# Kernel tuning notes

Measured on AMD Instinct MI355X. Metric: run time of the kernel, lower is better.

Reference implementation:

```python
import jax, jax.numpy as jnp
import numpy as np

SR = 16000
NUM_MEL = 80
FRAME_LEN = 400
FRAME_SHIFT = 160
PADDED_WIN = 512         # next pow2 of 400
NUM_FFT_BINS = PADDED_WIN // 2 + 1  # 257
PREEMPH = 0.97
EPS = 1e-6


def _mel_scale(f):
    return 1127.0 * np.log(1.0 + f / 700.0)


def _get_mel_banks(num_bins, window_padded, sample_freq, low_freq=20.0, high_freq=0.0):
    # Faithful port of torchaudio.compliance.kaldi.get_mel_banks (vtln_warp=1.0)
    num_fft_bins = window_padded // 2  # 256 (last bin padded with zero later)
    nyquist = 0.5 * sample_freq
    if high_freq <= 0.0:
        high_freq = nyquist + high_freq
    fft_bin_width = sample_freq / window_padded
    mel_low = _mel_scale(low_freq)
    mel_high = _mel_scale(high_freq)
    mel_delta = (mel_high - mel_low) / (num_bins + 1)
    left = mel_low + np.arange(num_bins, dtype=np.float64)[:, None] * mel_delta
    center = left + mel_delta
    right = center + mel_delta
    mel = _mel_scale(fft_bin_width * np.arange(num_fft_bins, dtype=np.float64))[None, :]
    up = (mel - left) / (center - left)
    down = (right - mel) / (right - center)
    bins = np.maximum(0.0, np.minimum(up, down))
    return bins.astype(np.float32)  # [num_bins, window_padded//2]


def _make_buffers():
    n = np.arange(FRAME_LEN, dtype=np.float32)
    window = (0.54 - 0.46 * np.cos(2 * np.pi * n / (FRAME_LEN - 1))).astype(np.float32)
    t = np.arange(PADDED_WIN, dtype=np.float32)
    f = np.arange(NUM_FFT_BINS, dtype=np.float32)[:, None]
    angles = 2.0 * np.pi * f * t / PADDED_WIN
    dft_real = np.cos(angles).astype(np.float32)        # [257, 512]
    dft_imag = (-np.sin(angles)).astype(np.float32)     # [257, 512]
    mel = _get_mel_banks(NUM_MEL, PADDED_WIN, float(SR))
    mel_weight = np.pad(mel, ((0, 0), (0, 1)))          # [80, 257]
    return window, dft_real, dft_imag, mel_weight


def setup_inputs() -> dict:
    key = jax.random.key(0)
    waveform = jax.random.normal(key, (32, 480000), dtype=jnp.float32)
    window, dft_real, dft_imag, mel_weight = _make_buffers()
    return {
        "waveform": waveform,
        "window": jnp.asarray(window),
        "dft_real": jnp.asarray(dft_real),
        "dft_imag": jnp.asarray(dft_imag),
        "mel_weight": jnp.asarray(mel_weight),
    }


def reference(waveform, window, dft_real, dft_imag, mel_weight):
    B, T = waveform.shape
    num_frames = (T - FRAME_LEN) // FRAME_SHIFT + 1
    # Framing (equivalent to conv1d with identity kernel, stride=FRAME_SHIFT)
    idx = jnp.arange(num_frames)[:, None] * FRAME_SHIFT + jnp.arange(FRAME_LEN)
    frames = waveform[:, idx].reshape(B * num_frames, FRAME_LEN)  # [BF, 400]
    # dither == 0 -> skipped
    # remove DC offset
    frames = frames - jnp.mean(frames, axis=1, keepdims=True)
    # raw energy (computed by the original module; unused since use_energy=False)
    _log_energy = jnp.log(jnp.maximum(jnp.sum(frames * frames, axis=1), EPS))
    # preemphasis with replicate left pad
    prev = jnp.concatenate([frames[:, :1], frames[:, :-1]], axis=1)
    frames = frames - PREEMPH * prev
    # Hamming window + zero pad to 512
    frames = frames * window[None, :]
    frames = jnp.pad(frames, ((0, 0), (0, PADDED_WIN - FRAME_LEN)))  # [BF, 512]
    # Brute-force DFT as matmuls
    real = frames @ dft_real.T  # [BF, 257]
    imag = frames @ dft_imag.T  # [BF, 257]
    power = real * real + imag * imag
    # Mel projection + log
    mel = power @ mel_weight.T + EPS  # [BF, 80]
    mel = jnp.log(jnp.maximum(mel, EPS))
    return mel.reshape(B, num_frames, NUM_MEL)
```

## Files before the change

### kernel.cpp

```cpp
#include <hip/hip_runtime.h>
#include <math.h>


#define BATCH 32
#define TLEN 480000
#define NFRAMES 2998
#define FL 400
#define FS 160
#define PW 512
#define NM 80
#define MT 32
#define NTILES 94
#define PRE 0.97f
#define EPSF 1e-6f

#define RE_KS 9
#define IM_KS 8
#define RE_U16 (16 * RE_KS * 64 * 8)
#define IM_U16 (16 * IM_KS * 64 * 8)
#define MEL_U16 (6 * 8 * 64 * 8)
#define OFF_REH 0
#define OFF_REL RE_U16
#define OFF_IMH (2 * RE_U16)
#define OFF_IML (2 * RE_U16 + IM_U16)
#define OFF_MEL (2 * RE_U16 + 2 * IM_U16)
#define WS_NEED ((size_t)(OFF_MEL + MEL_U16) * 2)

#define C0_SH 0
#define C0_SL 8704
#define C0_DH 17408
#define C0_DL 26112
#define C1_SH 0
#define C1_SL 10240
#define C1_DH 20480
#define C1_DL 29184

typedef short bf16x8 __attribute__((ext_vector_type(8)));
typedef float f32x4 __attribute__((ext_vector_type(4)));
typedef unsigned int u32;
typedef unsigned short u16;
typedef u32 u32x4 __attribute__((ext_vector_type(4)));

__device__ __forceinline__ u16 f2bf(float f) {
    u32 u = __builtin_bit_cast(u32, f);
    return (u16)((u + 0x7FFFu + ((u >> 16) & 1u)) >> 16);
}
__device__ __forceinline__ float bf2f(u16 h) {
    u32 u = ((u32)h) << 16;
    return __builtin_bit_cast(float, u);
}

__global__ void prep_kernel(const float* __restrict__ dftr, const float* __restrict__ dfti,
                            const float* __restrict__ melw, u16* __restrict__ wsb) {
    int idx = blockIdx.x * 256 + threadIdx.x;
    if (idx < 16 * RE_KS * 64) {
        int nf = idx / (RE_KS * 64);
        int rem = idx - nf * (RE_KS * 64);
        int ks = rem >> 6, l = rem & 63;
        int f = nf * 16 + (l & 15);
        int k = ks * 32 + ((l >> 4) << 3);
        u16* dh = wsb + OFF_REH + (size_t)idx * 8;
        u16* dl = wsb + OFF_REL + (size_t)idx * 8;
        #pragma unroll
        for (int e = 0; e < 8; ++e) {
            int kk = k + e;
            float x = (kk <= 256) ? dftr[(size_t)f * PW + kk] : 0.f;
            u16 h = f2bf(x);
            dh[e] = h;
            dl[e] = f2bf(x - bf2f(h));
        }
    } else if (idx < 16 * RE_KS * 64 + 16 * IM_KS * 64) {
        int j = idx - 16 * RE_KS * 64;
        int nf = j / (IM_KS * 64);
        int rem = j - nf * (IM_KS * 64);
        int ks = rem >> 6, l = rem & 63;
        int f = nf * 16 + (l & 15);
        int k = ks * 32 + ((l >> 4) << 3);
        u16* dh = wsb + OFF_IMH + (size_t)j * 8;
        u16* dl = wsb + OFF_IML + (size_t)j * 8;
        #pragma unroll
        for (int e = 0; e < 8; ++e) {
            float x = dfti[(size_t)f * PW + k + e];
            u16 h = f2bf(x);
            dh[e] = h;
            dl[e] = f2bf(x - bf2f(h));
        }
    } else {
        int m = idx - (16 * RE_KS * 64 + 16 * IM_KS * 64);
        if (m < 6 * 8 * 64) {
            int nf = m / (8 * 64);
            int ks = (m >> 6) & 7, l = m & 63;
            int n = nf * 16 + (l & 15);
            int k = ks * 32 + ((l >> 4) << 3);
            u16* dst = wsb + OFF_MEL + (size_t)m * 8;
            #pragma unroll
            for (int e = 0; e < 8; ++e)
                dst[e] = (n < NM) ? f2bf(melw[(size_t)n * 257 + k + e]) : (u16)0;
        }
    }
}

__device__ __forceinline__ u32 swz(int SWT, u32 r) {
    return (SWT == 0) ? ((r & 7u) << 4) : (SWT == 1) ? (((r >> 1) & 3u) << 4) : 0u;
}

#define MFMA6(D, J)                                                                        \
    _Pragma("unroll")                                                                      \
    for (int mf = 0; mf < 2; ++mf) {                                                       \
        acc[mf][J] = __builtin_amdgcn_mfma_f32_16x16x32_bf16(aH[mf], D[0], acc[mf][J], 0, 0, 0); \
        acc[mf][J] = __builtin_amdgcn_mfma_f32_16x16x32_bf16(aL[mf], D[0], acc[mf][J], 0, 0, 0); \
        acc[mf][J] = __builtin_amdgcn_mfma_f32_16x16x32_bf16(aH[mf], D[1], acc[mf][J], 0, 0, 0); \
    }

template<int RS, int SWT, int NKS, int BKS>
__device__ __forceinline__ void dft_pass(
    const char* tH, const char* tL,
    const u16* __restrict__ bH, const u16* __restrict__ bL,
    int ks0, int g, int lane, f32x4 (&acc)[2][4]) {

    bf16x8 aH[2], aL[2], Ba[2], Bb[2];

#define LDA_P(KS)                                                              \
    { _Pragma("unroll")                                                        \
      for (int mf = 0; mf < 2; ++mf) {                                         \
        u32 r = (u32)(mf * 16 + (lane & 15));                                  \
        u32 off = (u32)((KS) * 64 + ((lane >> 4) << 4));                       \
        u32 byte = r * RS + (off ^ swz(SWT, r));                               \
        aH[mf] = *(const bf16x8*)(tH + byte);                                  \
        aL[mf] = *(const bf16x8*)(tL + byte);                                  \
      } }
#define LDB_P(KSG, J, D)                                                       \
    {                                                                          \
        size_t o = ((size_t)((4 * g + (J)) * BKS + (KSG)) * 64 + lane) * 8;    \
        D[0] = *(const bf16x8*)(bH + o);                                       \
        D[1] = *(const bf16x8*)(bL + o);                                       \
    }

    LDB_P(ks0, 0, Ba);
    #pragma unroll
    for (int ks = 0; ks < NKS; ++ks) {
        LDA_P(ks);
        LDB_P(ks0 + ks, 1, Bb);
        MFMA6(Ba, 0);
        LDB_P(ks0 + ks, 2, Ba);
        MFMA6(Bb, 1);
        LDB_P(ks0 + ks, 3, Bb);
        MFMA6(Ba, 2);
        if (ks + 1 < NKS) LDB_P(ks0 + ks + 1, 0, Ba);
        MFMA6(Bb, 3);
    }
#undef LDA_P
#undef LDB_P
}

__device__ __forceinline__ void pack_write(const float* ys, char* baseH, char* baseL, u32 byte) {
    u32x4 hv, lv;
    #pragma unroll
    for (int e = 0; e < 4; ++e) {
        u16 h0 = f2bf(ys[2 * e]), h1 = f2bf(ys[2 * e + 1]);
        hv[e] = (u32)h0 | ((u32)h1 << 16);
        u16 l0 = f2bf(ys[2 * e] - bf2f(h0)), l1 = f2bf(ys[2 * e + 1] - bf2f(h1));
        lv[e] = (u32)l0 | ((u32)l1 << 16);
    }
    *(u32x4*)(baseH + byte) = hv;
    *(u32x4*)(baseL + byte) = lv;
}

__global__ __launch_bounds__(256, 3) void fbank_mfma(
    const float* __restrict__ wave, const float* __restrict__ win,
    const u16* __restrict__ wsb, float* __restrict__ out) {
    __shared__ float smean[MT];
    __shared__ u16 stile[18944];
    char* T = (char*)stile;

    const int tid = threadIdx.x, w = tid >> 6, lane = tid & 63;
    const int q = lane >> 4;
    const int cg = lane & 15;
    const int b = blockIdx.y;
    const int f0 = blockIdx.x * MT;
    const float* wb = wave + (size_t)b * TLEN;
    const float4* win4 = (const float4*)win;

    float mean[2];
    #pragma unroll
    for (int i = 0; i < 2; ++i) {
        const int rr = w * 8 + i * 4 + q;
        const int fr = f0 + rr;
        float acc = 0.f;
        if (fr < NFRAMES) {
            const float4* x4 = (const float4*)(wb + (size_t)fr * FS);
            #pragma unroll
            for (int m = 0; m < 6; ++m) {
                float4 a = x4[cg + 16 * m];
                acc += a.x + a.y + a.z + a.w;
            }
            if (cg < 4) { float4 a = x4[96 + cg]; acc += a.x + a.y + a.z + a.w; }
        }
        #pragma unroll
        for (int o = 8; o; o >>= 1) acc += __shfl_xor(acc, o);
        mean[i] = acc * (1.0f / FL);
        if (cg == 0) smean[rr] = mean[i];
    }

    #pragma unroll
    for (int i = 0; i < 2; ++i) {
        const int rr = w * 8 + i * 4 + q;
        const int fr = f0 + rr;
        const bool valid = fr < NFRAMES;
        const float* x = wb + (size_t)fr * FS;
        const float4* x4 = (const float4*)x;
        const float mc = (1.0f - PRE) * mean[i];

        float4 v0 = {0,0,0,0}, v1 = {0,0,0,0};
        if (valid) { v0 = x4[2 * cg]; v1 = x4[2 * cg + 1]; }
        float4 w0 = win4[2 * cg], w1 = win4[2 * cg + 1];
        float xpn = __shfl(v1.w, lane - 1);
        float xprev = (cg == 0) ? v0.x : xpn;
        float y[8];
        y[0] = (v0.x - PRE * xprev - mc) * w0.x;
        y[1] = (v0.y - PRE * v0.x - mc) * w0.y;
        y[2] = (v0.z - PRE * v0.y - mc) * w0.z;
        y[3] = (v0.w - PRE * v0.z - mc) * w0.w;
        y[4] = (v1.x - PRE * v0.w - mc) * w1.x;
        y[5] = (v1.y - PRE * v1.x - mc) * w1.y;
        y[6] = (v1.z - PRE * v1.y - mc) * w1.z;
        y[7] = (v1.w - PRE * v1.z - mc) * w1.w;

        float yr[8];
        #pragma unroll
        for (int e = 0; e < 8; ++e) yr[e] = 0.f;
        if (cg >= 14) {
            const int u0 = 512 - 8 * cg;
            float4 xr0 = {0,0,0,0}, xr1 = {0,0,0,0};
            float xu0 = 0.f;
            if (valid) {
                xr0 = x4[u0 / 4 - 2]; xr1 = x4[u0 / 4 - 1];
                if (u0 <= 399) xu0 = x[u0];
            }
            float4 wr0 = win4[u0 / 4 - 2], wr1 = win4[u0 / 4 - 1];
            float wu0 = (u0 <= 399) ? win[u0] : 0.f;
            yr[0] = (xu0   - PRE * xr1.w - mc) * wu0;
            yr[1] = (xr1.w - PRE * xr1.z - mc) * wr1.w;
            yr[2] = (xr1.z - PRE * xr1.y - mc) * wr1.z;
            yr[3] = (xr1.y - PRE * xr1.x - mc) * wr1.y;
            yr[4] = (xr1.x - PRE * xr0.w - mc) * wr1.x;
            yr[5] = (xr0.w - PRE * xr0.z - mc) * wr0.w;
            yr[6] = (xr0.z - PRE * xr0.y - mc) * wr0.z;
            yr[7] = (xr0.y - PRE * xr0.x - mc) * wr0.y;
        }
        float s8[8], d8[8];
        #pragma unroll
        for (int e = 0; e < 8; ++e) { s8[e] = y[e] + yr[e]; d8[e] = y[e] - yr[e]; }
        u32 byte = (u32)rr * 272u + (u32)cg * 16u;
        pack_write(s8, T + C0_SH, T + C0_SL, byte);
        pack_write(d8, T + C0_DH, T + C0_DL, byte);
    }
    __syncthreads();

    const int g = w;
    f32x4 accR[2][4], accI[2][4];
    #pragma unroll
    for (int mf = 0; mf < 2; ++mf)
        #pragma unroll
        for (int j = 0; j < 4; ++j) { accR[mf][j] = (f32x4)0.f; accI[mf][j] = (f32x4)0.f; }

    dft_pass<272, 2, 4, RE_KS>(T + C0_SH, T + C0_SL, wsb + OFF_REH, wsb + OFF_REL, 0, g, lane, accR);
    dft_pass<272, 2, 4, IM_KS>(T + C0_DH, T + C0_DL, wsb + OFF_IMH, wsb + OFF_IML, 0, g, lane, accI);
    __syncthreads();

    #pragma unroll
    for (int i = 0; i < 2; ++i) {
        const int rr = w * 8 + i * 4 + q;
        const int fr = f0 + rr;
        const bool valid = fr < NFRAMES;
        const float* x = wb + (size_t)fr * FS;
        const float4* x4 = (const float4*)x;
        const float mc = (1.0f - PRE) * mean[i];

        float4 v0 = {0,0,0,0}, v1 = {0,0,0,0};
        if (valid) { v0 = x4[32 + 2 * cg]; v1 = x4[33 + 2 * cg]; }
        float4 w0 = win4[32 + 2 * cg], w1 = win4[33 + 2 * cg];
        float xpn = __shfl(v1.w, lane - 1);
        float xprev = (cg == 0) ? (valid ? x[127] : 0.f) : xpn;
        float y[8];
        y[0] = (v0.x - PRE * xprev - mc) * w0.x;
        y[1] = (v0.y - PRE * v0.x - mc) * w0.y;
        y[2] = (v0.z - PRE * v0.y - mc) * w0.z;
        y[3] = (v0.w - PRE * v0.z - mc) * w0.w;
        y[4] = (v1.x - PRE * v0.w - mc) * w1.x;
        y[5] = (v1.y - PRE * v1.x - mc) * w1.y;
        y[6] = (v1.z - PRE * v1.y - mc) * w1.z;
        y[7] = (v1.w - PRE * v1.z - mc) * w1.w;

        const int u0 = 384 - 8 * cg;
        float4 xr0 = {0,0,0,0}, xr1 = {0,0,0,0};
        float xu0 = 0.f;
        if (valid) { xr0 = x4[u0 / 4 - 2]; xr1 = x4[u0 / 4 - 1]; xu0 = x[u0]; }
        float4 wr0 = win4[u0 / 4 - 2], wr1 = win4[u0 / 4 - 1];
        float wu0 = win[u0];
        float yr[8];
        yr[0] = (xu0   - PRE * xr1.w - mc) * wu0;
        yr[1] = (xr1.w - PRE * xr1.z - mc) * wr1.w;
        yr[2] = (xr1.z - PRE * xr1.y - mc) * wr1.z;
        yr[3] = (xr1.y - PRE * xr1.x - mc) * wr1.y;
        yr[4] = (xr1.x - PRE * xr0.w - mc) * wr1.x;
        yr[5] = (xr0.w - PRE * xr0.z - mc) * wr0.w;
        yr[6] = (xr0.z - PRE * xr0.y - mc) * wr0.z;
        yr[7] = (xr0.y - PRE * xr0.x - mc) * wr0.y;

        float s8[8], d8[8];
        #pragma unroll
        for (int e = 0; e < 8; ++e) { s8[e] = y[e] + yr[e]; d8[e] = y[e] - yr[e]; }
        u32 byteS = (u32)rr * 320u + (((u32)cg * 16u) ^ ((((u32)rr >> 1) & 3u) << 4));
        u32 byteD = (u32)rr * 272u + (u32)cg * 16u;
        pack_write(s8, T + C1_SH, T + C1_SL, byteS);
        pack_write(d8, T + C1_DH, T + C1_DL, byteD);
    }
    {
        const int rr = tid & 31;
        const int grp = tid >> 5;
        if (grp < 4) {
            const int fr = f0 + rr;
            float y256 = 0.f;
            if (grp == 0 && fr < NFRAMES) {
                const float* x = wb + (size_t)fr * FS;
                y256 = (x[256] - PRE * x[255] - (1.0f - PRE) * smean[rr]) * win[256];
            }
            float s8[8] = {y256, 0.f, 0.f, 0.f, 0.f, 0.f, 0.f, 0.f};
            u32 byte = (u32)rr * 320u + ((((u32)(16 + grp)) * 16u) ^ ((((u32)rr >> 1) & 3u) << 4));
            pack_write(s8, T + C1_SH, T + C1_SL, byte);
        }
    }
    __syncthreads();

    dft_pass<320, 1, 5, RE_KS>(T + C1_SH, T + C1_SL, wsb + OFF_REH, wsb + OFF_REL, 4, g, lane, accR);
    dft_pass<272, 2, 4, IM_KS>(T + C1_DH, T + C1_DL, wsb + OFF_IMH, wsb + OFF_IML, 4, g, lane, accI);
    __syncthreads();

    #pragma unroll
    for (int mf = 0; mf < 2; ++mf)
        #pragma unroll
        for (int j = 0; j < 4; ++j)
            #pragma unroll
            for (int r = 0; r < 4; ++r) {
                float pR = accR[mf][j][r], pI = accI[mf][j][r];
                float pw = pR * pR + pI * pI;
                u32 row = (u32)(mf * 16 + (q << 2) + r);
                u32 bin = (u32)(64 * g + j * 16 + cg);
                u32 byte = (row * 512u + bin * 2u) ^ ((row & 7u) << 4);
                *(u16*)(T + byte) = f2bf(pw);
            }
    __syncthreads();

    const u16* melb = wsb + OFF_MEL;
    {
        const int mfm = w >> 1;
        const int nf0 = (w & 1) ? 3 : 0;
        f32x4 accM[3];
        #pragma unroll
        for (int j = 0; j < 3; ++j) accM[j] = (f32x4)0.f;
        for (int ks = 0; ks < 8; ++ks) {
            u32 row = (u32)(mfm * 16 + cg);
            u32 byte = (row * 512u + (u32)(ks * 32 + (q << 3)) * 2u) ^ ((row & 7u) << 4);
            bf16x8 aP = *(const bf16x8*)(T + byte);
            #pragma unroll
            for (int j = 0; j < 3; ++j) {
                bf16x8 bM = *(const bf16x8*)(melb + ((size_t)((nf0 + j) * 8 + ks) * 64 + lane) * 8);
                accM[j] = __builtin_amdgcn_mfma_f32_16x16x32_bf16(aP, bM, accM[j], 0, 0, 0);
            }
        }
        #pragma unroll
        for (int j = 0; j < 3; ++j) {
            const int m = (nf0 + j) * 16 + cg;
            #pragma unroll
            for (int r = 0; r < 4; ++r) {
                const int rowl = mfm * 16 + (q << 2) + r;
                const int fr = f0 + rowl;
                if (fr < NFRAMES && m < NM) {
                    float v = fmaxf(accM[j][r] + EPSF, EPSF);
                    out[((size_t)b * NFRAMES + fr) * NM + m] = logf(v);
                }
            }
        }
    }
}

#define TFB 16
#define NB 256
__global__ __launch_bounds__(256, 3) void fbank_fallback(
    const float* __restrict__ wave, const float* __restrict__ win,
    const float* __restrict__ dftr, const float* __restrict__ dfti,
    const float* __restrict__ melw, float* __restrict__ out) {
    __shared__ float s_fr[TFB][PW];
    __shared__ float s_pw[TFB][NB + 1];
    const int tid = threadIdx.x, wv = tid >> 6, lane = tid & 63;
    const int fbase = blockIdx.x * TFB;
    #pragma unroll
    for (int j = 0; j < TFB / 4; ++j) {
        const int lf = wv * (TFB / 4) + j;
        const int gid = fbase + lf;
        const int bb = gid / NFRAMES;
        const int fr = gid - bb * NFRAMES;
        const float* x = wave + (size_t)bb * TLEN + (size_t)fr * FS;
        float s = 0.f;
        for (int i = lane; i < FL; i += 64) s += x[i];
        #pragma unroll
        for (int off = 32; off >= 1; off >>= 1) s += __shfl_xor(s, off);
        const float mean = s * (1.0f / FL);
        for (int i = lane; i < FL; i += 64) {
            const float xi = x[i];
            const float xm = (i == 0) ? xi : x[i - 1];
            s_fr[lf][i] = (xi - PRE * xm - (1.0f - PRE) * mean) * win[i];
        }
        for (int i = FL + lane; i < PW; i += 64) s_fr[lf][i] = 0.f;
    }
    __syncthreads();
    {
        const int bin = tid;
        const float4* dr4 = (const float4*)(dftr + (size_t)bin * PW);
        const float4* di4 = (const float4*)(dfti + (size_t)bin * PW);
        float accr[TFB], acci[TFB];
        #pragma unroll
        for (int f = 0; f < TFB; ++f) { accr[f] = 0.f; acci[f] = 0.f; }
        for (int k4 = 0; k4 < PW / 4; ++k4) {
            const float4 r = dr4[k4], im = di4[k4];
            #pragma unroll
            for (int f = 0; f < TFB; ++f) {
                const float4 fr = *(const float4*)&s_fr[f][k4 * 4];
                accr[f] += fr.x * r.x + fr.y * r.y + fr.z * r.z + fr.w * r.w;
                acci[f] += fr.x * im.x + fr.y * im.y + fr.z * im.z + fr.w * im.w;
            }
        }
        #pragma unroll
        for (int f = 0; f < TFB; ++f) s_pw[f][bin] = accr[f] * accr[f] + acci[f] * acci[f];
    }
    __syncthreads();
    for (int o = tid; o < TFB * NM; o += 256) {
        const int f = o / NM, m = o - f * NM;
        const float* wm = melw + (size_t)m * 257;
        float acc = 0.f;
        for (int k = 0; k < NB; ++k) acc += s_pw[f][k] * wm[k];
        out[(size_t)(fbase + f) * NM + m] = logf(fmaxf(acc + EPSF, EPSF));
    }
}

extern "C" void kernel_launch(void* const* d_in, const int* in_sizes, int n_in,
                              void* d_out, int out_size, void* d_ws, size_t ws_size,
                              hipStream_t stream) {
    const float* wave = (const float*)d_in[0];
    const float* win  = (const float*)d_in[1];
    const float* dftr = (const float*)d_in[2];
    const float* dfti = (const float*)d_in[3];
    const float* melw = (const float*)d_in[4];
    float* out = (float*)d_out;

    if (ws_size >= WS_NEED) {
        u16* wsb = (u16*)d_ws;
        const int prep_threads = 16 * RE_KS * 64 + 16 * IM_KS * 64 + 6 * 8 * 64;
        prep_kernel<<<(prep_threads + 255) / 256, 256, 0, stream>>>(dftr, dfti, melw, wsb);
        dim3 grid(NTILES, BATCH);
        fbank_mfma<<<grid, 256, 0, stream>>>(wave, win, wsb, out);
    } else {
        const int nblocks = (BATCH * NFRAMES) / TFB;
        fbank_fallback<<<nblocks, 256, 0, stream>>>(wave, win, dftr, dfti, melw, out);
    }
}
```

Measured before the change: 126.3 us.

## Apply DC-offset removal in frequency domain via precomputed window-DFT correction

Instead of a separate pass over each frame to compute the mean before preemphasis, the frame sum is accumulated from the samples already loaded for the DFT staging. Mean subtraction is applied after the DFT by subtracting mean times a precomputed DFT of the window, computed in the prep kernel. This removes a second global read of each frame before the DFT. In exchange, the prep kernel gains serial 257-term loops, and the subtraction of two large terms after the DFT may cost some precision.

```diff
diff --git a/kernel.cpp b/kernel.cpp
--- a/kernel.cpp
+++ b/kernel.cpp
@@ -24,7 +24,8 @@
 #define OFF_IMH (2 * RE_U16)
 #define OFF_IML (2 * RE_U16 + IM_U16)
 #define OFF_MEL (2 * RE_U16 + 2 * IM_U16)
-#define WS_NEED ((size_t)(OFF_MEL + MEL_U16) * 2)
+#define OFF_CS  (OFF_MEL + MEL_U16)
+#define WS_NEED ((size_t)OFF_CS * 2 + 512 * 4)
 
 #define C0_SH 0
 #define C0_SL 8704
@@ -51,7 +52,8 @@
 }
 
 __global__ void prep_kernel(const float* __restrict__ dftr, const float* __restrict__ dfti,
-                            const float* __restrict__ melw, u16* __restrict__ wsb) {
+                            const float* __restrict__ melw, const float* __restrict__ win,
+                            u16* __restrict__ wsb) {
     int idx = blockIdx.x * 256 + threadIdx.x;
     if (idx < 16 * RE_KS * 64) {
         int nf = idx / (RE_KS * 64);
@@ -85,17 +87,38 @@
             dh[e] = h;
             dl[e] = f2bf(x - bf2f(h));
         }
+    } else if (idx < 16 * RE_KS * 64 + 16 * IM_KS * 64 + 6 * 8 * 64) {
+        int m = idx - (16 * RE_KS * 64 + 16 * IM_KS * 64);
+        int nf = m / (8 * 64);
+        int ks = (m >> 6) & 7, l = m & 63;
+        int n = nf * 16 + (l & 15);
+        int k = ks * 32 + ((l >> 4) << 3);
+        u16* dst = wsb + OFF_MEL + (size_t)m * 8;
+        #pragma unroll
+        for (int e = 0; e < 8; ++e)
+            dst[e] = (n < NM) ? f2bf(melw[(size_t)n * 257 + k + e]) : (u16)0;
     } else {
-        int m = idx - (16 * RE_KS * 64 + 16 * IM_KS * 64);
-        if (m < 6 * 8 * 64) {
-            int nf = m / (8 * 64);
-            int ks = (m >> 6) & 7, l = m & 63;
-            int n = nf * 16 + (l & 15);
-            int k = ks * 32 + ((l >> 4) << 3);
-            u16* dst = wsb + OFF_MEL + (size_t)m * 8;
-            #pragma unroll
-            for (int e = 0; e < 8; ++e)
-                dst[e] = (n < NM) ? f2bf(melw[(size_t)n * 257 + k + e]) : (u16)0;
+        int f = idx - (16 * RE_KS * 64 + 16 * IM_KS * 64 + 6 * 8 * 64);
+        if (f < 512) {
+            float* cs = (float*)(wsb + OFF_CS);
+            if (f < 256) {
+                float acc = 0.f;
+                for (int t = 0; t <= 256; ++t) {
+                    float wt = (t < FL) ? win[t] : 0.f;
+                    float wu = (t >= 1 && t < 256 && (512 - t) < FL) ? win[512 - t] : 0.f;
+                    acc += (wt + wu) * dftr[(size_t)f * PW + t];
+                }
+                cs[f] = acc;
+            } else {
+                int ff = f - 256;
+                float acc = 0.f;
+                for (int t = 0; t <= 255; ++t) {
+                    float wt = (t < FL) ? win[t] : 0.f;
+                    float wu = (t >= 1 && (512 - t) < FL) ? win[512 - t] : 0.f;
+                    acc += (wt - wu) * dfti[(size_t)ff * PW + t];
+                }
+                cs[256 + ff] = acc;
+            }
         }
     }
 }
@@ -181,26 +204,7 @@
     const float* wb = wave + (size_t)b * TLEN;
     const float4* win4 = (const float4*)win;
 
-    float mean[2];
-    #pragma unroll
-    for (int i = 0; i < 2; ++i) {
-        const int rr = w * 8 + i * 4 + q;
-        const int fr = f0 + rr;
-        float acc = 0.f;
-        if (fr < NFRAMES) {
-            const float4* x4 = (const float4*)(wb + (size_t)fr * FS);
-            #pragma unroll
-            for (int m = 0; m < 6; ++m) {
-                float4 a = x4[cg + 16 * m];
-                acc += a.x + a.y + a.z + a.w;
-            }
-            if (cg < 4) { float4 a = x4[96 + cg]; acc += a.x + a.y + a.z + a.w; }
-        }
-        #pragma unroll
-        for (int o = 8; o; o >>= 1) acc += __shfl_xor(acc, o);
-        mean[i] = acc * (1.0f / FL);
-        if (cg == 0) smean[rr] = mean[i];
-    }
+    float ps[2] = {0.f, 0.f};
 
     #pragma unroll
     for (int i = 0; i < 2; ++i) {
@@ -209,22 +213,22 @@
         const bool valid = fr < NFRAMES;
         const float* x = wb + (size_t)fr * FS;
         const float4* x4 = (const float4*)x;
-        const float mc = (1.0f - PRE) * mean[i];
 
         float4 v0 = {0,0,0,0}, v1 = {0,0,0,0};
         if (valid) { v0 = x4[2 * cg]; v1 = x4[2 * cg + 1]; }
+        ps[i] += v0.x + v0.y + v0.z + v0.w + v1.x + v1.y + v1.z + v1.w;
         float4 w0 = win4[2 * cg], w1 = win4[2 * cg + 1];
         float xpn = __shfl(v1.w, lane - 1);
         float xprev = (cg == 0) ? v0.x : xpn;
         float y[8];
-        y[0] = (v0.x - PRE * xprev - mc) * w0.x;
-        y[1] = (v0.y - PRE * v0.x - mc) * w0.y;
-        y[2] = (v0.z - PRE * v0.y - mc) * w0.z;
-        y[3] = (v0.w - PRE * v0.z - mc) * w0.w;
-        y[4] = (v1.x - PRE * v0.w - mc) * w1.x;
-        y[5] = (v1.y - PRE * v1.x - mc) * w1.y;
-        y[6] = (v1.z - PRE * v1.y - mc) * w1.z;
-        y[7] = (v1.w - PRE * v1.z - mc) * w1.w;
+        y[0] = (v0.x - PRE * xprev) * w0.x;
+        y[1] = (v0.y - PRE * v0.x) * w0.y;
+        y[2] = (v0.z - PRE * v0.y) * w0.z;
+        y[3] = (v0.w - PRE * v0.z) * w0.w;
+        y[4] = (v1.x - PRE * v0.w) * w1.x;
+        y[5] = (v1.y - PRE * v1.x) * w1.y;
+        y[6] = (v1.z - PRE * v1.y) * w1.z;
+        y[7] = (v1.w - PRE * v1.z) * w1.w;
 
         float yr[8];
         #pragma unroll
@@ -237,16 +241,17 @@
                 xr0 = x4[u0 / 4 - 2]; xr1 = x4[u0 / 4 - 1];
                 if (u0 <= 399) xu0 = x[u0];
             }
+            ps[i] += xr0.x + xr0.y + xr0.z + xr0.w + xr1.x + xr1.y + xr1.z + xr1.w;
             float4 wr0 = win4[u0 / 4 - 2], wr1 = win4[u0 / 4 - 1];
             float wu0 = (u0 <= 399) ? win[u0] : 0.f;
-            yr[0] = (xu0   - PRE * xr1.w - mc) * wu0;
-            yr[1] = (xr1.w - PRE * xr1.z - mc) * wr1.w;
-            yr[2] = (xr1.z - PRE * xr1.y - mc) * wr1.z;
-            yr[3] = (xr1.y - PRE * xr1.x - mc) * wr1.y;
-            yr[4] = (xr1.x - PRE * xr0.w - mc) * wr1.x;
-            yr[5] = (xr0.w - PRE * xr0.z - mc) * wr0.w;
-            yr[6] = (xr0.z - PRE * xr0.y - mc) * wr0.z;
-            yr[7] = (xr0.y - PRE * xr0.x - mc) * wr0.y;
+            yr[0] = (xu0   - PRE * xr1.w) * wu0;
+            yr[1] = (xr1.w - PRE * xr1.z) * wr1.w;
+            yr[2] = (xr1.z - PRE * xr1.y) * wr1.z;
+            yr[3] = (xr1.y - PRE * xr1.x) * wr1.y;
+            yr[4] = (xr1.x - PRE * xr0.w) * wr1.x;
+            yr[5] = (xr0.w - PRE * xr0.z) * wr0.w;
+            yr[6] = (xr0.z - PRE * xr0.y) * wr0.z;
+            yr[7] = (xr0.y - PRE * xr0.x) * wr0.y;
         }
         float s8[8], d8[8];
         #pragma unroll
@@ -275,38 +280,39 @@
         const bool valid = fr < NFRAMES;
         const float* x = wb + (size_t)fr * FS;
         const float4* x4 = (const float4*)x;
-        const float mc = (1.0f - PRE) * mean[i];
 
         float4 v0 = {0,0,0,0}, v1 = {0,0,0,0};
         if (valid) { v0 = x4[32 + 2 * cg]; v1 = x4[33 + 2 * cg]; }
+        ps[i] += v0.x + v0.y + v0.z + v0.w + v1.x + v1.y + v1.z + v1.w;
         float4 w0 = win4[32 + 2 * cg], w1 = win4[33 + 2 * cg];
         float xpn = __shfl(v1.w, lane - 1);
         float xprev = (cg == 0) ? (valid ? x[127] : 0.f) : xpn;
         float y[8];
-        y[0] = (v0.x - PRE * xprev - mc) * w0.x;
-        y[1] = (v0.y - PRE * v0.x - mc) * w0.y;
-        y[2] = (v0.z - PRE * v0.y - mc) * w0.z;
-        y[3] = (v0.w - PRE * v0.z - mc) * w0.w;
-        y[4] = (v1.x - PRE * v0.w - mc) * w1.x;
-        y[5] = (v1.y - PRE * v1.x - mc) * w1.y;
-        y[6] = (v1.z - PRE * v1.y - mc) * w1.z;
-        y[7] = (v1.w - PRE * v1.z - mc) * w1.w;
+        y[0] = (v0.x - PRE * xprev) * w0.x;
+        y[1] = (v0.y - PRE * v0.x) * w0.y;
+        y[2] = (v0.z - PRE * v0.y) * w0.z;
+        y[3] = (v0.w - PRE * v0.z) * w0.w;
+        y[4] = (v1.x - PRE * v0.w) * w1.x;
+        y[5] = (v1.y - PRE * v1.x) * w1.y;
+        y[6] = (v1.z - PRE * v1.y) * w1.z;
+        y[7] = (v1.w - PRE * v1.z) * w1.w;
 
         const int u0 = 384 - 8 * cg;
         float4 xr0 = {0,0,0,0}, xr1 = {0,0,0,0};
         float xu0 = 0.f;
         if (valid) { xr0 = x4[u0 / 4 - 2]; xr1 = x4[u0 / 4 - 1]; xu0 = x[u0]; }
+        ps[i] += xr0.x + xr0.y + xr0.z + xr0.w + xr1.x + xr1.y + xr1.z + xr1.w;
         float4 wr0 = win4[u0 / 4 - 2], wr1 = win4[u0 / 4 - 1];
         float wu0 = win[u0];
         float yr[8];
-        yr[0] = (xu0   - PRE * xr1.w - mc) * wu0;
-        yr[1] = (xr1.w - PRE * xr1.z - mc) * wr1.w;
-        yr[2] = (xr1.z - PRE * xr1.y - mc) * wr1.z;
-        yr[3] = (xr1.y - PRE * xr1.x - mc) * wr1.y;
-        yr[4] = (xr1.x - PRE * xr0.w - mc) * wr1.x;
-        yr[5] = (xr0.w - PRE * xr0.z - mc) * wr0.w;
-        yr[6] = (xr0.z - PRE * xr0.y - mc) * wr0.z;
-        yr[7] = (xr0.y - PRE * xr0.x - mc) * wr0.y;
+        yr[0] = (xu0   - PRE * xr1.w) * wu0;
+        yr[1] = (xr1.w - PRE * xr1.z) * wr1.w;
+        yr[2] = (xr1.z - PRE * xr1.y) * wr1.z;
+        yr[3] = (xr1.y - PRE * xr1.x) * wr1.y;
+        yr[4] = (xr1.x - PRE * xr0.w) * wr1.x;
+        yr[5] = (xr0.w - PRE * xr0.z) * wr0.w;
+        yr[6] = (xr0.z - PRE * xr0.y) * wr0.z;
+        yr[7] = (xr0.y - PRE * xr0.x) * wr0.y;
 
         float s8[8], d8[8];
         #pragma unroll
@@ -315,6 +321,11 @@
         u32 byteD = (u32)rr * 272u + (u32)cg * 16u;
         pack_write(s8, T + C1_SH, T + C1_SL, byteS);
         pack_write(d8, T + C1_DH, T + C1_DL, byteD);
+
+        float acc = ps[i];
+        #pragma unroll
+        for (int o = 8; o; o >>= 1) acc += __shfl_xor(acc, o);
+        if (cg == 0) smean[rr] = acc * (1.0f / FL);
     }
     {
         const int rr = tid & 31;
@@ -324,7 +335,7 @@
             float y256 = 0.f;
             if (grp == 0 && fr < NFRAMES) {
                 const float* x = wb + (size_t)fr * FS;
-                y256 = (x[256] - PRE * x[255] - (1.0f - PRE) * smean[rr]) * win[256];
+                y256 = (x[256] - PRE * x[255]) * win[256];
             }
             float s8[8] = {y256, 0.f, 0.f, 0.f, 0.f, 0.f, 0.f, 0.f};
             u32 byte = (u32)rr * 320u + ((((u32)(16 + grp)) * 16u) ^ ((((u32)rr >> 1) & 3u) << 4));
@@ -337,19 +348,26 @@
     dft_pass<272, 2, 4, IM_KS>(T + C1_DH, T + C1_DL, wsb + OFF_IMH, wsb + OFF_IML, 4, g, lane, accI);
     __syncthreads();
 
-    #pragma unroll
-    for (int mf = 0; mf < 2; ++mf)
-        #pragma unroll
-        for (int j = 0; j < 4; ++j)
+    {
+        const float* cs = (const float*)(wsb + OFF_CS);
+        #pragma unroll
+        for (int mf = 0; mf < 2; ++mf)
             #pragma unroll
-            for (int r = 0; r < 4; ++r) {
-                float pR = accR[mf][j][r], pI = accI[mf][j][r];
-                float pw = pR * pR + pI * pI;
-                u32 row = (u32)(mf * 16 + (q << 2) + r);
-                u32 bin = (u32)(64 * g + j * 16 + cg);
-                u32 byte = (row * 512u + bin * 2u) ^ ((row & 7u) << 4);
-                *(u16*)(T + byte) = f2bf(pw);
-            }
+            for (int j = 0; j < 4; ++j) {
+                const u32 bin = (u32)(64 * g + j * 16 + cg);
+                const float Cb = cs[bin], Sb = cs[256 + bin];
+                #pragma unroll
+                for (int r = 0; r < 4; ++r) {
+                    u32 row = (u32)(mf * 16 + (q << 2) + r);
+                    const float mcr = (1.0f - PRE) * smean[row];
+                    float pR = accR[mf][j][r] - mcr * Cb;
+                    float pI = accI[mf][j][r] - mcr * Sb;
+                    float pw = pR * pR + pI * pI;
+                    u32 byte = (row * 512u + bin * 2u) ^ ((row & 7u) << 4);
+                    *(u16*)(T + byte) = f2bf(pw);
+                }
+            }
+    }
     __syncthreads();
 
     const u16* melb = wsb + OFF_MEL;
@@ -456,8 +474,8 @@
 
     if (ws_size >= WS_NEED) {
         u16* wsb = (u16*)d_ws;
-        const int prep_threads = 16 * RE_KS * 64 + 16 * IM_KS * 64 + 6 * 8 * 64;
-        prep_kernel<<<(prep_threads + 255) / 256, 256, 0, stream>>>(dftr, dfti, melw, wsb);
+        const int prep_threads = 16 * RE_KS * 64 + 16 * IM_KS * 64 + 6 * 8 * 64 + 512;
+        prep_kernel<<<(prep_threads + 255) / 256, 256, 0, stream>>>(dftr, dfti, melw, win, wsb);
         dim3 grid(NTILES, BATCH);
         fbank_mfma<<<grid, 256, 0, stream>>>(wave, win, wsb, out);
     } else {
```

Result: slower. 154.1 us (+22.0%).
